# Kernel tuning notes

Measured on AMD Instinct MI355X. Metric: run time of the kernel, lower is better.

## Reference

```python
import math
import jax, jax.numpy as jnp
import numpy as np

B, Q, K = 1, 2048, 2048
CQ = CK = CV = 128
H, CH = 8, 32
HD = H * CH  # 256


def setup_inputs() -> dict:
    key = jax.random.key(0)
    ks = jax.random.split(key, 12)
    s = 0.02
    return {
        "q_x": jax.random.normal(ks[0], (B, Q, CQ), jnp.float32),
        "kv_x": jax.random.normal(ks[1], (B, K, CK), jnp.float32),
        "bias": jax.random.normal(ks[2], (B, 1, Q, K), jnp.float32),
        "distance": jax.random.uniform(ks[3], (B, Q, K, H), jnp.float32),
        "Wq": jax.random.normal(ks[4], (CQ, HD), jnp.float32) * s,
        "Wk": jax.random.normal(ks[5], (CK, HD), jnp.float32) * s,
        "Wv": jax.random.normal(ks[6], (CV, HD), jnp.float32) * s,
        "Wg": jax.random.normal(ks[7], (CQ, HD), jnp.float32) * s,
        "bg": jnp.zeros((HD,), jnp.float32),
        "Wo": jax.random.normal(ks[8], (HD, CQ), jnp.float32) * s,
        "bo": jnp.zeros((CQ,), jnp.float32),
    }


def reference(q_x, kv_x, bias, distance, Wq, Wk, Wv, Wg, bg, Wo, bo):
    # Projections -> [B, S, H, CH]
    q = (q_x @ Wq).reshape(B, Q, H, CH) / math.sqrt(CH)
    k = (kv_x @ Wk).reshape(B, K, H, CH)
    v = (kv_x @ Wv).reshape(B, K, H, CH)
    # Scores [B, H, Q, K]
    a = jnp.einsum("bqhc,bkhc->bhqk", q, k)
    a = a + bias
    # mha_permu=True: distance [B,Q,K,H] -> [B,H,Q,K]; rel_dis_pair_bias='add'
    a = a + jnp.transpose(distance, (0, 3, 1, 2))
    a = jax.nn.softmax(a, axis=-1)
    o = jnp.einsum("bhqk,bkhc->bqhc", a, v)  # [B, Q, H, CH]
    # Gating
    g = jax.nn.sigmoid(q_x @ Wg + bg).reshape(B, Q, H, CH)
    o = o * g
    o = o.reshape(B, Q, HD)
    return o @ Wo + bo
```

## Files before the change

### kernel.cpp

```cpp
#include <hip/hip_runtime.h>
#include <hip/hip_bf16.h>

#define Qn 2048
#define Kn 2048
#define Cin 128
#define Hn 8
#define CHn 32
#define HDn 256

typedef __attribute__((ext_vector_type(8))) short short8;
typedef __attribute__((ext_vector_type(4))) float f32x4;

static __device__ __forceinline__ unsigned short f2bf(float f) {
    unsigned int u = __float_as_uint(f);
    u += 0x7fffu + ((u >> 16) & 1u);
    return (unsigned short)(u >> 16);
}

__global__ __launch_bounds__(256) void proj_kernel(
    const float* __restrict__ qx, const float* __restrict__ kvx,
    const float* __restrict__ Wq, const float* __restrict__ Wk,
    const float* __restrict__ Wv, const float* __restrict__ Wg,
    const float* __restrict__ bg,
    unsigned short* __restrict__ qb, unsigned short* __restrict__ kb,
    unsigned short* __restrict__ vtb, float* __restrict__ gb)
{
    const int mat = blockIdx.y;
    const int r0 = blockIdx.x * 4;
    const int j = threadIdx.x;
    const float* A = (mat == 0 || mat == 3) ? qx : kvx;
    const float* W = (mat == 0) ? Wq : (mat == 1) ? Wk : (mat == 2) ? Wv : Wg;
    const float* Ar = A + r0 * Cin;
    float a0 = 0.f, a1 = 0.f, a2 = 0.f, a3 = 0.f;
    for (int c = 0; c < Cin; ++c) {
        const float w = W[c * HDn + j];
        a0 = fmaf(Ar[c], w, a0);
        a1 = fmaf(Ar[Cin + c], w, a1);
        a2 = fmaf(Ar[2 * Cin + c], w, a2);
        a3 = fmaf(Ar[3 * Cin + c], w, a3);
    }
    if (mat == 0) {
        const float s = 0.17677669529663687f;
        qb[(r0 + 0) * HDn + j] = f2bf(a0 * s);
        qb[(r0 + 1) * HDn + j] = f2bf(a1 * s);
        qb[(r0 + 2) * HDn + j] = f2bf(a2 * s);
        qb[(r0 + 3) * HDn + j] = f2bf(a3 * s);
    } else if (mat == 1) {
        kb[(r0 + 0) * HDn + j] = f2bf(a0);
        kb[(r0 + 1) * HDn + j] = f2bf(a1);
        kb[(r0 + 2) * HDn + j] = f2bf(a2);
        kb[(r0 + 3) * HDn + j] = f2bf(a3);
    } else if (mat == 2) {
        vtb[j * Kn + r0 + 0] = f2bf(a0);
        vtb[j * Kn + r0 + 1] = f2bf(a1);
        vtb[j * Kn + r0 + 2] = f2bf(a2);
        vtb[j * Kn + r0 + 3] = f2bf(a3);
    } else {
        const float b = bg[j];
        gb[(r0 + 0) * HDn + j] = 1.f / (1.f + __expf(-(a0 + b)));
        gb[(r0 + 1) * HDn + j] = 1.f / (1.f + __expf(-(a1 + b)));
        gb[(r0 + 2) * HDn + j] = 1.f / (1.f + __expf(-(a2 + b)));
        gb[(r0 + 3) * HDn + j] = 1.f / (1.f + __expf(-(a3 + b)));
    }
}

__global__ __launch_bounds__(512) void attn_kernel(
    const unsigned short* __restrict__ qb, const unsigned short* __restrict__ kb,
    const unsigned short* __restrict__ vtb,
    const float* __restrict__ bias, const float* __restrict__ dist,
    float* __restrict__ opart, float* __restrict__ mlpart)
{
    __shared__ unsigned short ps[Hn][16][72];
    const int bx = blockIdx.x;
    const int qt = bx >> 1;
    const int ks = bx & 1;
    const int q0 = qt * 16;
    const int k00 = ks * 1024;
    const int tid = threadIdx.x;
    const int h = tid >> 6;
    const int l = tid & 63;
    const int g = l >> 4;
    const int n = l & 15;

    const short8 qf = *(const short8*)(qb + (q0 + n) * HDn + h * CHn + g * 8);

    f32x4 o0 = {0.f, 0.f, 0.f, 0.f};
    f32x4 o1 = {0.f, 0.f, 0.f, 0.f};
    float mreg[4] = {-__builtin_inff(), -__builtin_inff(), -__builtin_inff(), -__builtin_inff()};
    float lreg[4] = {0.f, 0.f, 0.f, 0.f};
    unsigned short* psh = &ps[h][0][0];
    const f32x4 z = {0.f, 0.f, 0.f, 0.f};

    for (int kt = 0; kt < 16; ++kt) {
        const int k0 = k00 + kt * 64;
        f32x4 sf[4];
        #pragma unroll
        for (int kkg = 0; kkg < 4; ++kkg) {
            const short8 kf = *(const short8*)(kb + (k0 + kkg * 16 + n) * HDn + h * CHn + g * 8);
            sf[kkg] = __builtin_amdgcn_mfma_f32_16x16x32_bf16(qf, kf, z, 0, 0, 0);
        }
        #pragma unroll
        for (int kkg = 0; kkg < 4; ++kkg) {
            #pragma unroll
            for (int r = 0; r < 4; ++r) {
                const int qg = q0 + g * 4 + r;
                const int kg = k0 + kkg * 16 + n;
                sf[kkg][r] += bias[qg * Kn + kg] + dist[(qg * Kn + kg) * Hn + h];
            }
        }
        #pragma unroll
        for (int r = 0; r < 4; ++r) {
            float v = fmaxf(fmaxf(sf[0][r], sf[1][r]), fmaxf(sf[2][r], sf[3][r]));
            v = fmaxf(v, __shfl_xor(v, 1));
            v = fmaxf(v, __shfl_xor(v, 2));
            v = fmaxf(v, __shfl_xor(v, 4));
            v = fmaxf(v, __shfl_xor(v, 8));
            const float mnew = fmaxf(mreg[r], v);
            const float alpha = __expf(mreg[r] - mnew);
            mreg[r] = mnew;
            const float p0 = __expf(sf[0][r] - mnew);
            const float p1 = __expf(sf[1][r] - mnew);
            const float p2 = __expf(sf[2][r] - mnew);
            const float p3 = __expf(sf[3][r] - mnew);
            sf[0][r] = p0; sf[1][r] = p1; sf[2][r] = p2; sf[3][r] = p3;
            float rs = p0 + p1 + p2 + p3;
            rs += __shfl_xor(rs, 1);
            rs += __shfl_xor(rs, 2);
            rs += __shfl_xor(rs, 4);
            rs += __shfl_xor(rs, 8);
            lreg[r] = lreg[r] * alpha + rs;
            o0[r] *= alpha;
            o1[r] *= alpha;
        }
        #pragma unroll
        for (int kkg = 0; kkg < 4; ++kkg) {
            #pragma unroll
            for (int r = 0; r < 4; ++r)
                psh[(g * 4 + r) * 72 + kkg * 16 + n] = f2bf(sf[kkg][r]);
        }
        #pragma unroll
        for (int chunk = 0; chunk < 2; ++chunk) {
            const short8 pf = *(const short8*)(psh + n * 72 + chunk * 32 + g * 8);
            const short8 vf0 = *(const short8*)(vtb + (h * CHn + n) * Kn + k0 + chunk * 32 + g * 8);
            o0 = __builtin_amdgcn_mfma_f32_16x16x32_bf16(pf, vf0, o0, 0, 0, 0);
            const short8 vf1 = *(const short8*)(vtb + (h * CHn + 16 + n) * Kn + k0 + chunk * 32 + g * 8);
            o1 = __builtin_amdgcn_mfma_f32_16x16x32_bf16(pf, vf1, o1, 0, 0, 0);
        }
    }
    float* op = opart + ks * (Qn * HDn);
    #pragma unroll
    for (int r = 0; r < 4; ++r) {
        const int qg = q0 + g * 4 + r;
        op[qg * HDn + h * CHn + n] = o0[r];
        op[qg * HDn + h * CHn + 16 + n] = o1[r];
    }
    if (n == 0) {
        float* ml = mlpart + ks * (Qn * Hn * 2);
        #pragma unroll
        for (int r = 0; r < 4; ++r) {
            const int qg = q0 + g * 4 + r;
            ml[(qg * Hn + h) * 2 + 0] = mreg[r];
            ml[(qg * Hn + h) * 2 + 1] = lreg[r];
        }
    }
}

__global__ __launch_bounds__(256) void merge_kernel(
    const float* __restrict__ opart, const float* __restrict__ mlpart,
    const float* __restrict__ gb, float* __restrict__ ob)
{
    const int q = blockIdx.x;
    const int j = threadIdx.x;
    const int h = j >> 5;
    const float m0 = mlpart[(q * Hn + h) * 2 + 0];
    const float l0 = mlpart[(q * Hn + h) * 2 + 1];
    const float m1 = mlpart[Qn * Hn * 2 + (q * Hn + h) * 2 + 0];
    const float l1 = mlpart[Qn * Hn * 2 + (q * Hn + h) * 2 + 1];
    const float mm = fmaxf(m0, m1);
    const float a0 = __expf(m0 - mm);
    const float a1 = __expf(m1 - mm);
    const float denom = l0 * a0 + l1 * a1;
    const float o = (opart[q * HDn + j] * a0 + opart[Qn * HDn + q * HDn + j] * a1) / denom;
    ob[q * HDn + j] = o * gb[q * HDn + j];
}

__global__ __launch_bounds__(128) void outproj_kernel(
    const float* __restrict__ ob, const float* __restrict__ Wo,
    const float* __restrict__ bo, float* __restrict__ out)
{
    const int r0 = blockIdx.x * 4;
    const int j = threadIdx.x;
    const float* Or = ob + r0 * HDn;
    float a0 = 0.f, a1 = 0.f, a2 = 0.f, a3 = 0.f;
    for (int c = 0; c < HDn; ++c) {
        const float w = Wo[c * Cin + j];
        a0 = fmaf(Or[c], w, a0);
        a1 = fmaf(Or[HDn + c], w, a1);
        a2 = fmaf(Or[2 * HDn + c], w, a2);
        a3 = fmaf(Or[3 * HDn + c], w, a3);
    }
    const float b = bo[j];
    out[(r0 + 0) * Cin + j] = a0 + b;
    out[(r0 + 1) * Cin + j] = a1 + b;
    out[(r0 + 2) * Cin + j] = a2 + b;
    out[(r0 + 3) * Cin + j] = a3 + b;
}

extern "C" void kernel_launch(void* const* d_in, const int* in_sizes, int n_in,
                              void* d_out, int out_size, void* d_ws, size_t ws_size,
                              hipStream_t stream)
{
    const float* qx   = (const float*)d_in[0];
    const float* kvx  = (const float*)d_in[1];
    const float* bias = (const float*)d_in[2];
    const float* dist = (const float*)d_in[3];
    const float* Wq   = (const float*)d_in[4];
    const float* Wk   = (const float*)d_in[5];
    const float* Wv   = (const float*)d_in[6];
    const float* Wg   = (const float*)d_in[7];
    const float* bg   = (const float*)d_in[8];
    const float* Wo   = (const float*)d_in[9];
    const float* bo   = (const float*)d_in[10];
    float* out = (float*)d_out;

    char* w = (char*)d_ws;
    unsigned short* qb  = (unsigned short*)(w);
    unsigned short* kb  = (unsigned short*)(w + (1u << 20));
    unsigned short* vtb = (unsigned short*)(w + (2u << 20));
    float* gb     = (float*)(w + (3u << 20));
    float* opart  = (float*)(w + (5u << 20));
    float* mlpart = (float*)(w + (9u << 20));
    float* ob     = (float*)(w + (10u << 20));

    proj_kernel<<<dim3(Qn / 4, 4), 256, 0, stream>>>(qx, kvx, Wq, Wk, Wv, Wg, bg, qb, kb, vtb, gb);
    attn_kernel<<<dim3(256), 512, 0, stream>>>(qb, kb, vtb, bias, dist, opart, mlpart);
    merge_kernel<<<dim3(Qn), 256, 0, stream>>>(opart, mlpart, gb, ob);
    outproj_kernel<<<dim3(Qn / 4), 128, 0, stream>>>(ob, Wo, bo, out);
}
```

Baseline: 323.6 us.

## Pre-transpose bias+distance to fp16, drop online max, split K 8 ways, fuse merge/outproj

```diff
diff --git a/kernel.cpp b/kernel.cpp
--- a/kernel.cpp
+++ b/kernel.cpp
@@ -7,6 +7,8 @@
 #define Hn 8
 #define CHn 32
 #define HDn 256
+#define QK (Qn * Kn)
+#define NSPLIT 8
 
 typedef __attribute__((ext_vector_type(8))) short short8;
 typedef __attribute__((ext_vector_type(4))) float f32x4;
@@ -26,56 +28,81 @@
     unsigned short* __restrict__ vtb, float* __restrict__ gb)
 {
     const int mat = blockIdx.y;
-    const int r0 = blockIdx.x * 4;
+    const int r0 = blockIdx.x * 8;
     const int j = threadIdx.x;
     const float* A = (mat == 0 || mat == 3) ? qx : kvx;
     const float* W = (mat == 0) ? Wq : (mat == 1) ? Wk : (mat == 2) ? Wv : Wg;
     const float* Ar = A + r0 * Cin;
-    float a0 = 0.f, a1 = 0.f, a2 = 0.f, a3 = 0.f;
+    float acc[8] = {0.f, 0.f, 0.f, 0.f, 0.f, 0.f, 0.f, 0.f};
     for (int c = 0; c < Cin; ++c) {
         const float w = W[c * HDn + j];
-        a0 = fmaf(Ar[c], w, a0);
-        a1 = fmaf(Ar[Cin + c], w, a1);
-        a2 = fmaf(Ar[2 * Cin + c], w, a2);
-        a3 = fmaf(Ar[3 * Cin + c], w, a3);
+        #pragma unroll
+        for (int i = 0; i < 8; ++i)
+            acc[i] = fmaf(Ar[i * Cin + c], w, acc[i]);
     }
     if (mat == 0) {
         const float s = 0.17677669529663687f;
-        qb[(r0 + 0) * HDn + j] = f2bf(a0 * s);
-        qb[(r0 + 1) * HDn + j] = f2bf(a1 * s);
-        qb[(r0 + 2) * HDn + j] = f2bf(a2 * s);
-        qb[(r0 + 3) * HDn + j] = f2bf(a3 * s);
+        #pragma unroll
+        for (int i = 0; i < 8; ++i)
+            qb[(r0 + i) * HDn + j] = f2bf(acc[i] * s);
     } else if (mat == 1) {
-        kb[(r0 + 0) * HDn + j] = f2bf(a0);
-        kb[(r0 + 1) * HDn + j] = f2bf(a1);
-        kb[(r0 + 2) * HDn + j] = f2bf(a2);
-        kb[(r0 + 3) * HDn + j] = f2bf(a3);
+        #pragma unroll
+        for (int i = 0; i < 8; ++i)
+            kb[(r0 + i) * HDn + j] = f2bf(acc[i]);
     } else if (mat == 2) {
-        vtb[j * Kn + r0 + 0] = f2bf(a0);
-        vtb[j * Kn + r0 + 1] = f2bf(a1);
-        vtb[j * Kn + r0 + 2] = f2bf(a2);
-        vtb[j * Kn + r0 + 3] = f2bf(a3);
+        unsigned short tmp[8];
+        #pragma unroll
+        for (int i = 0; i < 8; ++i) tmp[i] = f2bf(acc[i]);
+        *(short8*)(vtb + (size_t)j * Kn + r0) = *(short8*)tmp;
     } else {
         const float b = bg[j];
-        gb[(r0 + 0) * HDn + j] = 1.f / (1.f + __expf(-(a0 + b)));
-        gb[(r0 + 1) * HDn + j] = 1.f / (1.f + __expf(-(a1 + b)));
-        gb[(r0 + 2) * HDn + j] = 1.f / (1.f + __expf(-(a2 + b)));
-        gb[(r0 + 3) * HDn + j] = 1.f / (1.f + __expf(-(a3 + b)));
-    }
-}
-
+        #pragma unroll
+        for (int i = 0; i < 8; ++i)
+            gb[(r0 + i) * HDn + j] = 1.f / (1.f + __expf(-(acc[i] + b)));
+    }
+}
+
+__global__ __launch_bounds__(256) void prepass_kernel(
+    const float* __restrict__ bias, const float* __restrict__ dist,
+    _Float16* __restrict__ db)
+{
+    __shared__ _Float16 lds[Hn * 272];
+    const int q = blockIdx.x;
+    const int k0 = blockIdx.y * 256;
+    const int t = threadIdx.x;
+    const float b = bias[q * Kn + k0 + t];
+    const float4* dp = (const float4*)(dist + (size_t)(q * Kn + k0 + t) * Hn);
+    const float4 d0 = dp[0];
+    const float4 d1 = dp[1];
+    lds[0 * 272 + t] = (_Float16)(d0.x + b);
+    lds[1 * 272 + t] = (_Float16)(d0.y + b);
+    lds[2 * 272 + t] = (_Float16)(d0.z + b);
+    lds[3 * 272 + t] = (_Float16)(d0.w + b);
+    lds[4 * 272 + t] = (_Float16)(d1.x + b);
+    lds[5 * 272 + t] = (_Float16)(d1.y + b);
+    lds[6 * 272 + t] = (_Float16)(d1.z + b);
+    lds[7 * 272 + t] = (_Float16)(d1.w + b);
+    __syncthreads();
+    const int h = t >> 5;
+    const int c8 = (t & 31) * 8;
+    const short8 v = *(const short8*)(lds + h * 272 + c8);
+    *(short8*)((unsigned short*)db + (size_t)h * QK + (size_t)q * Kn + k0 + c8) = v;
+}
+
+template <bool USE_DB>
 __global__ __launch_bounds__(512) void attn_kernel(
     const unsigned short* __restrict__ qb, const unsigned short* __restrict__ kb,
     const unsigned short* __restrict__ vtb,
+    const _Float16* __restrict__ db,
     const float* __restrict__ bias, const float* __restrict__ dist,
-    float* __restrict__ opart, float* __restrict__ mlpart)
+    float* __restrict__ opart, float* __restrict__ lpart)
 {
     __shared__ unsigned short ps[Hn][16][72];
     const int bx = blockIdx.x;
-    const int qt = bx >> 1;
-    const int ks = bx & 1;
+    const int qt = bx >> 3;
+    const int sp = bx & 7;
     const int q0 = qt * 16;
-    const int k00 = ks * 1024;
+    const int k00 = sp * 256;
     const int tid = threadIdx.x;
     const int h = tid >> 6;
     const int l = tid & 63;
@@ -83,54 +110,44 @@
     const int n = l & 15;
 
     const short8 qf = *(const short8*)(qb + (q0 + n) * HDn + h * CHn + g * 8);
+    const _Float16* dbh = db + (size_t)h * QK;
 
     f32x4 o0 = {0.f, 0.f, 0.f, 0.f};
     f32x4 o1 = {0.f, 0.f, 0.f, 0.f};
-    float mreg[4] = {-__builtin_inff(), -__builtin_inff(), -__builtin_inff(), -__builtin_inff()};
-    float lreg[4] = {0.f, 0.f, 0.f, 0.f};
+    float lacc[4] = {0.f, 0.f, 0.f, 0.f};
     unsigned short* psh = &ps[h][0][0];
     const f32x4 z = {0.f, 0.f, 0.f, 0.f};
 
-    for (int kt = 0; kt < 16; ++kt) {
+    for (int kt = 0; kt < 4; ++kt) {
         const int k0 = k00 + kt * 64;
-        f32x4 sf[4];
-        #pragma unroll
-        for (int kkg = 0; kkg < 4; ++kkg) {
-            const short8 kf = *(const short8*)(kb + (k0 + kkg * 16 + n) * HDn + h * CHn + g * 8);
-            sf[kkg] = __builtin_amdgcn_mfma_f32_16x16x32_bf16(qf, kf, z, 0, 0, 0);
-        }
+        float dbv[4][4];
         #pragma unroll
         for (int kkg = 0; kkg < 4; ++kkg) {
             #pragma unroll
             for (int r = 0; r < 4; ++r) {
                 const int qg = q0 + g * 4 + r;
                 const int kg = k0 + kkg * 16 + n;
-                sf[kkg][r] += bias[qg * Kn + kg] + dist[(qg * Kn + kg) * Hn + h];
+                if (USE_DB)
+                    dbv[kkg][r] = (float)dbh[(size_t)qg * Kn + kg];
+                else
+                    dbv[kkg][r] = bias[(size_t)qg * Kn + kg] +
+                                  dist[((size_t)qg * Kn + kg) * Hn + h];
             }
         }
-        #pragma unroll
-        for (int r = 0; r < 4; ++r) {
-            float v = fmaxf(fmaxf(sf[0][r], sf[1][r]), fmaxf(sf[2][r], sf[3][r]));
-            v = fmaxf(v, __shfl_xor(v, 1));
-            v = fmaxf(v, __shfl_xor(v, 2));
-            v = fmaxf(v, __shfl_xor(v, 4));
-            v = fmaxf(v, __shfl_xor(v, 8));
-            const float mnew = fmaxf(mreg[r], v);
-            const float alpha = __expf(mreg[r] - mnew);
-            mreg[r] = mnew;
-            const float p0 = __expf(sf[0][r] - mnew);
-            const float p1 = __expf(sf[1][r] - mnew);
-            const float p2 = __expf(sf[2][r] - mnew);
-            const float p3 = __expf(sf[3][r] - mnew);
-            sf[0][r] = p0; sf[1][r] = p1; sf[2][r] = p2; sf[3][r] = p3;
-            float rs = p0 + p1 + p2 + p3;
-            rs += __shfl_xor(rs, 1);
-            rs += __shfl_xor(rs, 2);
-            rs += __shfl_xor(rs, 4);
-            rs += __shfl_xor(rs, 8);
-            lreg[r] = lreg[r] * alpha + rs;
-            o0[r] *= alpha;
-            o1[r] *= alpha;
+        f32x4 sf[4];
+        #pragma unroll
+        for (int kkg = 0; kkg < 4; ++kkg) {
+            const short8 kf = *(const short8*)(kb + (k0 + kkg * 16 + n) * HDn + h * CHn + g * 8);
+            sf[kkg] = __builtin_amdgcn_mfma_f32_16x16x32_bf16(qf, kf, z, 0, 0, 0);
+        }
+        #pragma unroll
+        for (int kkg = 0; kkg < 4; ++kkg) {
+            #pragma unroll
+            for (int r = 0; r < 4; ++r) {
+                const float p = __expf(sf[kkg][r] + dbv[kkg][r]);
+                sf[kkg][r] = p;
+                lacc[r] += p;
+            }
         }
         #pragma unroll
         for (int kkg = 0; kkg < 4; ++kkg) {
@@ -147,63 +164,61 @@
             o1 = __builtin_amdgcn_mfma_f32_16x16x32_bf16(pf, vf1, o1, 0, 0, 0);
         }
     }
-    float* op = opart + ks * (Qn * HDn);
+    float* op = opart + (size_t)sp * (Qn * HDn);
     #pragma unroll
     for (int r = 0; r < 4; ++r) {
         const int qg = q0 + g * 4 + r;
         op[qg * HDn + h * CHn + n] = o0[r];
         op[qg * HDn + h * CHn + 16 + n] = o1[r];
+        float v = lacc[r];
+        v += __shfl_xor(v, 1);
+        v += __shfl_xor(v, 2);
+        v += __shfl_xor(v, 4);
+        v += __shfl_xor(v, 8);
+        lacc[r] = v;
     }
     if (n == 0) {
-        float* ml = mlpart + ks * (Qn * Hn * 2);
-        #pragma unroll
-        for (int r = 0; r < 4; ++r) {
-            const int qg = q0 + g * 4 + r;
-            ml[(qg * Hn + h) * 2 + 0] = mreg[r];
-            ml[(qg * Hn + h) * 2 + 1] = lreg[r];
-        }
-    }
-}
-
-__global__ __launch_bounds__(256) void merge_kernel(
-    const float* __restrict__ opart, const float* __restrict__ mlpart,
-    const float* __restrict__ gb, float* __restrict__ ob)
-{
+        float* lp = lpart + (size_t)sp * (Qn * Hn);
+        #pragma unroll
+        for (int r = 0; r < 4; ++r)
+            lp[(q0 + g * 4 + r) * Hn + h] = lacc[r];
+    }
+}
+
+__global__ __launch_bounds__(256) void mergeout_kernel(
+    const float* __restrict__ opart, const float* __restrict__ lpart,
+    const float* __restrict__ gb, const float* __restrict__ Wo,
+    const float* __restrict__ bo, float* __restrict__ out)
+{
+    __shared__ float olds[HDn];
+    __shared__ float red[4][128];
     const int q = blockIdx.x;
-    const int j = threadIdx.x;
-    const int h = j >> 5;
-    const float m0 = mlpart[(q * Hn + h) * 2 + 0];
-    const float l0 = mlpart[(q * Hn + h) * 2 + 1];
-    const float m1 = mlpart[Qn * Hn * 2 + (q * Hn + h) * 2 + 0];
-    const float l1 = mlpart[Qn * Hn * 2 + (q * Hn + h) * 2 + 1];
-    const float mm = fmaxf(m0, m1);
-    const float a0 = __expf(m0 - mm);
-    const float a1 = __expf(m1 - mm);
-    const float denom = l0 * a0 + l1 * a1;
-    const float o = (opart[q * HDn + j] * a0 + opart[Qn * HDn + q * HDn + j] * a1) / denom;
-    ob[q * HDn + j] = o * gb[q * HDn + j];
-}
-
-__global__ __launch_bounds__(128) void outproj_kernel(
-    const float* __restrict__ ob, const float* __restrict__ Wo,
-    const float* __restrict__ bo, float* __restrict__ out)
-{
-    const int r0 = blockIdx.x * 4;
-    const int j = threadIdx.x;
-    const float* Or = ob + r0 * HDn;
-    float a0 = 0.f, a1 = 0.f, a2 = 0.f, a3 = 0.f;
-    for (int c = 0; c < HDn; ++c) {
-        const float w = Wo[c * Cin + j];
-        a0 = fmaf(Or[c], w, a0);
-        a1 = fmaf(Or[HDn + c], w, a1);
-        a2 = fmaf(Or[2 * HDn + c], w, a2);
-        a3 = fmaf(Or[3 * HDn + c], w, a3);
-    }
-    const float b = bo[j];
-    out[(r0 + 0) * Cin + j] = a0 + b;
-    out[(r0 + 1) * Cin + j] = a1 + b;
-    out[(r0 + 2) * Cin + j] = a2 + b;
-    out[(r0 + 3) * Cin + j] = a3 + b;
+    const int t = threadIdx.x;
+    const int h = t >> 5;
+    float s = 0.f;
+    #pragma unroll
+    for (int sp = 0; sp < NSPLIT; ++sp)
+        s += opart[(size_t)sp * (Qn * HDn) + q * HDn + t];
+    float lt = 0.f;
+    #pragma unroll
+    for (int sp = 0; sp < NSPLIT; ++sp)
+        lt += lpart[(size_t)sp * (Qn * Hn) + q * Hn + h];
+    olds[t] = (s / lt) * gb[q * HDn + t];
+    __syncthreads();
+    const int p = t & 63;
+    const int seg = t >> 6;
+    float a0 = 0.f, a1 = 0.f;
+    for (int c = seg * 64; c < seg * 64 + 64; ++c) {
+        const float ov = olds[c];
+        const float2 w = *(const float2*)(Wo + c * Cin + 2 * p);
+        a0 = fmaf(ov, w.x, a0);
+        a1 = fmaf(ov, w.y, a1);
+    }
+    red[seg][2 * p] = a0;
+    red[seg][2 * p + 1] = a1;
+    __syncthreads();
+    if (t < 128)
+        out[q * Cin + t] = red[0][t] + red[1][t] + red[2][t] + red[3][t] + bo[t];
 }
 
 extern "C" void kernel_launch(void* const* d_in, const int* in_sizes, int n_in,
@@ -225,15 +240,20 @@
 
     char* w = (char*)d_ws;
     unsigned short* qb  = (unsigned short*)(w);
-    unsigned short* kb  = (unsigned short*)(w + (1u << 20));
-    unsigned short* vtb = (unsigned short*)(w + (2u << 20));
-    float* gb     = (float*)(w + (3u << 20));
-    float* opart  = (float*)(w + (5u << 20));
-    float* mlpart = (float*)(w + (9u << 20));
-    float* ob     = (float*)(w + (10u << 20));
-
-    proj_kernel<<<dim3(Qn / 4, 4), 256, 0, stream>>>(qx, kvx, Wq, Wk, Wv, Wg, bg, qb, kb, vtb, gb);
-    attn_kernel<<<dim3(256), 512, 0, stream>>>(qb, kb, vtb, bias, dist, opart, mlpart);
-    merge_kernel<<<dim3(Qn), 256, 0, stream>>>(opart, mlpart, gb, ob);
-    outproj_kernel<<<dim3(Qn / 4), 128, 0, stream>>>(ob, Wo, bo, out);
-}
+    unsigned short* kb  = (unsigned short*)(w + (1ull << 20));
+    unsigned short* vtb = (unsigned short*)(w + (2ull << 20));
+    float* gb    = (float*)(w + (3ull << 20));
+    float* opart = (float*)(w + (5ull << 20));
+    float* lpart = (float*)(w + (21ull << 20));
+    _Float16* db = (_Float16*)(w + (22ull << 20));
+    const size_t need_db = 86ull << 20;
+
+    proj_kernel<<<dim3(Qn / 8, 4), 256, 0, stream>>>(qx, kvx, Wq, Wk, Wv, Wg, bg, qb, kb, vtb, gb);
+    if (ws_size >= need_db) {
+        prepass_kernel<<<dim3(Qn, Kn / 256), 256, 0, stream>>>(bias, dist, db);
+        attn_kernel<true><<<dim3(128 * NSPLIT), 512, 0, stream>>>(qb, kb, vtb, db, bias, dist, opart, lpart);
+    } else {
+        attn_kernel<false><<<dim3(128 * NSPLIT), 512, 0, stream>>>(qb, kb, vtb, db, bias, dist, opart, lpart);
+    }
+    mergeout_kernel<<<dim3(Qn), 256, 0, stream>>>(opart, lpart, gb, Wo, bo, out);
+}
```

Measured after the change: 310.6 us. 1.04x faster.
